# Performance work log

Measured on AMD Instinct MI355X. Metric: run time of the kernel, lower is better.

The kernel has to match this reference:

```python
import jax, jax.numpy as jnp
import numpy as np

N_USER, N_ENTITY, N_NEWS, N_REL, K, D, NNZ = 50000, 60000, 20000, 50, 20, 100, 500000

def setup_inputs() -> dict:
    key = jax.random.key(0)
    ks = jax.random.split(key, 12)
    return {
        "user_emb": jax.random.normal(ks[0], (N_USER, D), jnp.float32),
        "all_embedding": jax.random.normal(ks[1], (N_ENTITY, D), jnp.float32),
        "entity_emb": jax.random.normal(ks[2], (N_ENTITY, D), jnp.float32),
        "relation_emb": jax.random.normal(ks[3], (N_REL, D), jnp.float32),
        "W_news": jax.random.normal(ks[4], (D, 1), jnp.float32) * 0.1,
        "b_news": jax.random.normal(ks[5], (1,), jnp.float32) * 0.1,
        "W_ent": jax.random.normal(ks[6], (D, 1), jnp.float32) * 0.1,
        "b_ent": jax.random.normal(ks[7], (1,), jnp.float32) * 0.1,
        "interact_vals": jax.random.uniform(ks[8], (NNZ,), jnp.float32),
        "news_entities": jax.random.randint(ks[9], (N_NEWS, K), 0, N_ENTITY, jnp.int32),
        "news_relations": jnp.zeros((N_NEWS, K), jnp.int32),  # original code hardcodes relation 0 for news
        "neigh_entities": jax.random.randint(ks[10], (N_ENTITY, K), 0, N_ENTITY, jnp.int32),
        "neigh_relations": jax.random.randint(ks[11], (N_ENTITY, K), 0, N_REL, jnp.int32),
        "interact_rows": jax.random.randint(jax.random.fold_in(key, 100), (NNZ,), 0, N_USER, jnp.int32),
        "interact_cols": jax.random.randint(jax.random.fold_in(key, 101), (NNZ,), 0, N_NEWS + N_ENTITY, jnp.int32),
    }

def reference(user_emb, all_embedding, entity_emb, relation_emb, W_news, b_news,
              W_ent, b_ent, interact_vals, news_entities, news_relations,
              neigh_entities, neigh_relations, interact_rows, interact_cols):
    n_news = news_entities.shape[0]
    n_entity = entity_emb.shape[0]
    n_user = user_emb.shape[0]

    # --- news aggregation: newsid = arange(N_NEWS) ---
    news_emb = all_embedding[:n_news]                              # [N_news, D]
    nne = entity_emb[news_entities]                                # [N_news, K, D]
    nnr = relation_emb[news_relations]                             # [N_news, K, D]
    news_logits = (nne + nnr) @ W_news + b_news                    # [N_news, K, 1]
    # faithful: softmax over last (size-1) dim -> all-ones weights
    news_w = jax.nn.softmax(news_logits, axis=-1)
    news_agg = jnp.einsum('nko,nkd->nd', news_w, nne)              # [N_news, D]

    # --- entity aggregation: entities = arange(n_entity); entity_emb overwritten ---
    ent_base = all_embedding[:n_entity]                            # [n_entity, D]
    ne = ent_base[neigh_entities]                                  # [n_entity, K, D]
    nr = relation_emb[neigh_relations]                             # [n_entity, K, D]
    ent_logits = (nr + ne) @ W_ent + b_ent                         # [n_entity, K, 1]
    ent_w = jax.nn.softmax(ent_logits, axis=-1)
    entity_agg = jnp.einsum('nko,nkd->nd', ent_w, ne)              # [n_entity, D]

    node_emb = jnp.concatenate([news_agg + news_emb, entity_agg + ent_base], axis=0)

    # --- sparse mm: interact_mat [n_user, n_news+n_entity] in COO ---
    gathered = interact_vals[:, None] * node_emb[interact_cols]    # [nnz, D]
    user_agg = jax.ops.segment_sum(gathered, interact_rows, num_segments=n_user)
    user_agg = user_emb + user_agg
    return node_emb, user_agg
```

## Files before the change

### kernel.cpp

```cpp
#include <hip/hip_runtime.h>
#include <hip/hip_bf16.h>

constexpr int D        = 100;
constexpr int K        = 20;
constexpr int N_USER   = 50000;
constexpr int N_ENTITY = 60000;
constexpr int N_NEWS   = 20000;
constexpr int NNZ      = 500000;
constexpr int CAP      = 32;
constexpr int N_NODE   = N_NEWS + N_ENTITY;
constexpr int FS       = 32;

constexpr int PREP_WAVES = N_ENTITY;
constexpr int PREP_ROWT  = PREP_WAVES * 64;

__global__ __launch_bounds__(256) void prep_kernel(
    const float* __restrict__ ent, const float* __restrict__ all,
    unsigned int* __restrict__ entQ, unsigned int* __restrict__ allQ,
    int* __restrict__ counts, int* __restrict__ listcnt)
{
    int i = (int)(blockIdx.x * blockDim.x + threadIdx.x);
    if (i < PREP_ROWT) {
        int w    = i >> 6;
        int lane = i & 63;
        int li   = lane & 31;
        int sub  = lane >> 5;
        bool isEnt = w < PREP_WAVES / 2;
        const float* src = isEnt ? ent : all;
        unsigned int* dst = isEnt ? entQ : allQ;
        int row = 2 * (isEnt ? w : (w - PREP_WAVES / 2)) + sub;

        float v0 = 0.f, v1 = 0.f, v2 = 0.f, v3 = 0.f, lmax = 0.f;
        if (li < 25) {
            const float* sp = src + (size_t)row * D + li * 4;
            v0 = __builtin_nontemporal_load(sp + 0);
            v1 = __builtin_nontemporal_load(sp + 1);
            v2 = __builtin_nontemporal_load(sp + 2);
            v3 = __builtin_nontemporal_load(sp + 3);
            lmax = fmaxf(fmaxf(fabsf(v0), fabsf(v1)),
                         fmaxf(fabsf(v2), fabsf(v3)));
        }
        #pragma unroll
        for (int off = 16; off >= 1; off >>= 1)
            lmax = fmaxf(lmax, __shfl_xor(lmax, off));

        float inv = (lmax > 0.f) ? (127.0f / lmax) : 0.f;
        unsigned int o = 0;
        if (li < 25) {
            int q0 = (int)rintf(v0 * inv);
            int q1 = (int)rintf(v1 * inv);
            int q2 = (int)rintf(v2 * inv);
            int q3 = (int)rintf(v3 * inv);
            o = ((unsigned int)(unsigned char)(signed char)q0)
              | ((unsigned int)(unsigned char)(signed char)q1 << 8)
              | ((unsigned int)(unsigned char)(signed char)q2 << 16)
              | ((unsigned int)(unsigned char)(signed char)q3 << 24);
        } else if (li == 25) {
            o = __float_as_uint(lmax * (1.0f / 127.0f));
        }
        dst[(size_t)row * FS + li] = o;
    } else {
        int j = i - PREP_ROWT;
        if (j < N_USER) counts[j] = 0;
        else if (j == N_USER) *listcnt = 0;
    }
}

static __device__ __forceinline__ void sumagg_body(
    const unsigned int* __restrict__ tabQ,
    const int*   __restrict__ idx_mat,
    const float* __restrict__ base,
    float*       __restrict__ node,
    unsigned int* __restrict__ nodeQ,
    int pair, int lane)
{
    int li   = lane & 31;
    int sub  = lane >> 5;
    int row  = pair * 2 + sub;

    int idxv = (li < K)
        ? __builtin_nontemporal_load(idx_mat + (size_t)row * K + li) : 0;

    unsigned int t[K];
    #pragma unroll
    for (int k = 0; k < K; ++k) {
        int col = __shfl(idxv, sub * 32 + k);
        t[k] = tabQ[(size_t)col * FS + li];
    }

    float a0 = 0.f, a1 = 0.f, a2 = 0.f, a3 = 0.f;
    #pragma unroll
    for (int k = 0; k < K; ++k) {
        float sc = __uint_as_float((unsigned int)__shfl((int)t[k], sub * 32 + 25));
        unsigned int u = t[k];
        a0 += (float)((signed char)(u       & 0xFF)) * sc;
        a1 += (float)((signed char)((u >> 8) & 0xFF)) * sc;
        a2 += (float)((signed char)((u >> 16) & 0xFF)) * sc;
        a3 += (float)((int)u >> 24) * sc;
    }

    float o0 = 0.f, o1 = 0.f, o2 = 0.f, o3 = 0.f, lmax = 0.f;
    if (li < 25) {
        const float* bp = base + (size_t)row * D + li * 4;
        o0 = a0 + __builtin_nontemporal_load(bp + 0);
        o1 = a1 + __builtin_nontemporal_load(bp + 1);
        o2 = a2 + __builtin_nontemporal_load(bp + 2);
        o3 = a3 + __builtin_nontemporal_load(bp + 3);
        float* np = node + (size_t)row * D + li * 4;
        __builtin_nontemporal_store(o0, np + 0);
        __builtin_nontemporal_store(o1, np + 1);
        __builtin_nontemporal_store(o2, np + 2);
        __builtin_nontemporal_store(o3, np + 3);
        lmax = fmaxf(fmaxf(fabsf(o0), fabsf(o1)),
                     fmaxf(fabsf(o2), fabsf(o3)));
    }
    #pragma unroll
    for (int off = 16; off >= 1; off >>= 1)
        lmax = fmaxf(lmax, __shfl_xor(lmax, off));
    float inv = (lmax > 0.f) ? (127.0f / lmax) : 0.f;

    unsigned int oq = 0;
    if (li < 25) {
        int q0 = (int)rintf(o0 * inv);
        int q1 = (int)rintf(o1 * inv);
        int q2 = (int)rintf(o2 * inv);
        int q3 = (int)rintf(o3 * inv);
        oq = ((unsigned int)(unsigned char)(signed char)q0)
           | ((unsigned int)(unsigned char)(signed char)q1 << 8)
           | ((unsigned int)(unsigned char)(signed char)q2 << 16)
           | ((unsigned int)(unsigned char)(signed char)q3 << 24);
    } else if (li == 25) {
        oq = __float_as_uint(lmax * (1.0f / 127.0f));
    }
    nodeQ[(size_t)row * FS + li] = oq;
}

static __device__ __forceinline__ void hist_body(
    const int* __restrict__ rows, const int* __restrict__ cols,
    const float* __restrict__ vals,
    int* __restrict__ counts, unsigned int* __restrict__ bpack,
    int* __restrict__ list, int* __restrict__ listcnt, int j)
{
    int r   = __builtin_nontemporal_load(rows + j);
    int pos = atomicAdd(&counts[r], 1);
    if (pos < CAP) {
        int   c = __builtin_nontemporal_load(cols + j);
        float v = __builtin_nontemporal_load(vals + j);
        int q = (int)(v * 32767.0f + 0.5f);
        if (q > 32767) q = 32767;
        if (q < 0) q = 0;
        bpack[(size_t)r * CAP + pos] = (unsigned int)c | ((unsigned int)q << 17);
    } else {
        int s = atomicAdd(listcnt, 1);
        list[s] = j;
    }
}

constexpr int NEWS_BLK = (N_NEWS / 2 + 3) / 4;
constexpr int HIST_BLK = (NNZ + 255) / 256;

__global__ __launch_bounds__(256) void news_hist_kernel(
    const unsigned int* __restrict__ entQ,
    const int*   __restrict__ news_ent,
    const float* __restrict__ base,
    float*       __restrict__ node,
    unsigned int* __restrict__ nodeQ,
    const int* __restrict__ irows, const int* __restrict__ icols,
    const float* __restrict__ vals,
    int* __restrict__ counts, unsigned int* __restrict__ bpack,
    int* __restrict__ list, int* __restrict__ listcnt)
{
    int b = (int)blockIdx.x;
    if (b < NEWS_BLK) {
        int pair = b * 4 + (int)(threadIdx.x >> 6);
        if (pair < N_NEWS / 2)
            sumagg_body(entQ, news_ent, base, node, nodeQ,
                        pair, (int)threadIdx.x & 63);
    } else {
        int j = (b - NEWS_BLK) * 256 + (int)threadIdx.x;
        if (j < NNZ)
            hist_body(irows, icols, vals, counts, bpack, list, listcnt, j);
    }
}

__global__ __launch_bounds__(256) void sumagg_q8_kernel(
    const unsigned int* __restrict__ tabQ,
    const int*   __restrict__ idx_mat,
    const float* __restrict__ base,
    float*       __restrict__ node,
    unsigned int* __restrict__ nodeQ,
    int n)
{
    int pair = (int)((blockIdx.x * blockDim.x + threadIdx.x) >> 6);
    if (pair >= (n >> 1)) return;
    sumagg_body(tabQ, idx_mat, base, node, nodeQ,
                pair, (int)threadIdx.x & 63);
}

__global__ __launch_bounds__(256) void user_agg_q8_kernel(
    const int* __restrict__ counts, const unsigned int* __restrict__ bpack,
    const unsigned int* __restrict__ nodeQ,
    const float* __restrict__ user_emb, float* __restrict__ user)
{
    int u    = (int)((blockIdx.x * blockDim.x + threadIdx.x) >> 6);
    int lane = threadIdx.x & 63;
    int li   = lane & 31;
    int sub  = lane >> 5;
    if (u >= N_USER) return;

    int c = counts[u];
    if (c > CAP) c = CAP;

    int colv = 0; float valv = 0.f;
    if (lane < c) {
        unsigned int pk = __builtin_nontemporal_load(bpack + (size_t)u * CAP + lane);
        colv = (int)(pk & 0x1FFFFu);
        valv = (float)(pk >> 17) * (1.0f / 32767.0f);
    }
    int clampi = (c > 0) ? (c - 1) : 0;
    int pairs  = (c + 1) >> 1;

    float a0 = 0.f, a1 = 0.f, a2 = 0.f, a3 = 0.f;
    for (int p0 = 0; p0 < pairs; p0 += 4) {
        unsigned int t[4]; float v[4];
        #pragma unroll
        for (int e = 0; e < 4; ++e) {
            int pe    = 2 * (p0 + e) + sub;
            bool valid = pe < c;
            int es    = valid ? pe : clampi;
            int   col = __shfl(colv, es);
            float vv  = __shfl(valv, es);
            v[e] = valid ? vv : 0.f;
            t[e] = nodeQ[(size_t)col * FS + li];
        }
        #pragma unroll
        for (int e = 0; e < 4; ++e) {
            float sc = __uint_as_float(
                (unsigned int)__shfl((int)t[e], sub * 32 + 25)) * v[e];
            unsigned int w = t[e];
            a0 += (float)((signed char)(w       & 0xFF)) * sc;
            a1 += (float)((signed char)((w >> 8) & 0xFF)) * sc;
            a2 += (float)((signed char)((w >> 16) & 0xFF)) * sc;
            a3 += (float)((int)w >> 24) * sc;
        }
    }
    a0 += __shfl_xor(a0, 32);
    a1 += __shfl_xor(a1, 32);
    a2 += __shfl_xor(a2, 32);
    a3 += __shfl_xor(a3, 32);

    if (sub == 0 && li < 25) {
        const float* up = user_emb + (size_t)u * D + li * 4;
        float u0 = __builtin_nontemporal_load(up + 0);
        float u1 = __builtin_nontemporal_load(up + 1);
        float u2 = __builtin_nontemporal_load(up + 2);
        float u3 = __builtin_nontemporal_load(up + 3);
        float* op = user + (size_t)u * D + li * 4;
        __builtin_nontemporal_store(a0 + u0, op + 0);
        __builtin_nontemporal_store(a1 + u1, op + 1);
        __builtin_nontemporal_store(a2 + u2, op + 2);
        __builtin_nontemporal_store(a3 + u3, op + 3);
    }
}

__global__ __launch_bounds__(256) void drain_kernel(
    const int* __restrict__ list, const int* __restrict__ listcnt,
    const int* __restrict__ rows, const int* __restrict__ cols,
    const float* __restrict__ vals, const float* __restrict__ node,
    float* __restrict__ user)
{
    int nw   = (int)((gridDim.x * blockDim.x) >> 6);
    int wid  = (int)((blockIdx.x * blockDim.x + threadIdx.x) >> 6);
    int lane = threadIdx.x & 63;
    int cnt  = *listcnt;
    if (cnt > NNZ) cnt = NNZ;
    for (int s = wid; s < cnt; s += nw) {
        int j = list[s];
        int   r = rows[j];
        int   c = cols[j];
        float v = vals[j];
        const float* src = node + (size_t)c * D;
        float*       dst = user + (size_t)r * D;
        unsafeAtomicAdd(&dst[lane], v * src[lane]);
        int l2 = lane + 64;
        if (l2 < D) unsafeAtomicAdd(&dst[l2], v * src[l2]);
    }
}

__global__ __launch_bounds__(256) void zero2_kernel(
    int* __restrict__ counts, int* __restrict__ listcnt, int n)
{
    int i = (int)(blockIdx.x * blockDim.x + threadIdx.x);
    if (i < n) counts[i] = 0;
    else if (i == n) *listcnt = 0;
}

__global__ __launch_bounds__(256) void hist_fill_kernel(
    const int* __restrict__ rows, const int* __restrict__ cols,
    const float* __restrict__ vals,
    int* __restrict__ counts, unsigned int* __restrict__ bpack,
    int* __restrict__ list, int* __restrict__ listcnt, int nnz)
{
    int j = (int)(blockIdx.x * blockDim.x + threadIdx.x);
    if (j >= nnz) return;
    hist_body(rows, cols, vals, counts, bpack, list, listcnt, j);
}

__global__ __launch_bounds__(256) void sumagg_f32_kernel(
    const float* __restrict__ table, const int* __restrict__ idx_mat,
    const float* __restrict__ base, float* __restrict__ out, int n)
{
    int wave = (int)((blockIdx.x * blockDim.x + threadIdx.x) >> 6);
    int lane = threadIdx.x & 63;
    if (wave >= n) return;
    int idxv = (lane < K) ? idx_mat[(size_t)wave * K + lane] : 0;
    float acc0 = 0.f, acc1 = 0.f;
    int l2 = lane + 64;
    #pragma unroll
    for (int k = 0; k < K; ++k) {
        int ei = __shfl(idxv, k);
        const float* r = table + (size_t)ei * D;
        acc0 += r[lane];
        if (l2 < D) acc1 += r[l2];
    }
    const float* b = base + (size_t)wave * D;
    float*       o = out  + (size_t)wave * D;
    o[lane] = acc0 + b[lane];
    if (l2 < D) o[l2] = acc1 + b[l2];
}

__global__ __launch_bounds__(256) void user_agg_f32_kernel(
    const int* __restrict__ counts, const unsigned int* __restrict__ bpack,
    const float* __restrict__ node,
    const float* __restrict__ user_emb, float* __restrict__ user)
{
    int u    = (int)((blockIdx.x * blockDim.x + threadIdx.x) >> 6);
    int lane = threadIdx.x & 63;
    if (u >= N_USER) return;
    int c = counts[u];
    if (c > CAP) c = CAP;
    int colv = 0; float valv = 0.f;
    if (lane < c) {
        unsigned int pk = bpack[(size_t)u * CAP + lane];
        colv = (int)(pk & 0x1FFFFu);
        valv = (float)(pk >> 17) * (1.0f / 32767.0f);
    }
    float a0 = 0.f, a1 = 0.f;
    int l2 = lane + 64;
    for (int e = 0; e < c; ++e) {
        int   col = __shfl(colv, e);
        float v   = __shfl(valv, e);
        const float* r = node + (size_t)col * D;
        a0 += v * r[lane];
        if (l2 < D) a1 += v * r[l2];
    }
    const float* ue = user_emb + (size_t)u * D;
    float*       o  = user     + (size_t)u * D;
    o[lane] = a0 + ue[lane];
    if (l2 < D) o[l2] = a1 + ue[l2];
}

__global__ __launch_bounds__(256) void copy_kernel(
    const float4* __restrict__ src, float4* __restrict__ dst, int n4)
{
    int i = (int)(blockIdx.x * blockDim.x + threadIdx.x);
    if (i < n4) dst[i] = src[i];
}

__global__ __launch_bounds__(256) void scatter_kernel(
    const float* __restrict__ vals, const int* __restrict__ rows,
    const int* __restrict__ cols, const float* __restrict__ node,
    float* __restrict__ user, int nnz)
{
    int j    = (int)((blockIdx.x * blockDim.x + threadIdx.x) >> 6);
    int lane = threadIdx.x & 63;
    if (j >= nnz) return;
    int   r = rows[j];
    int   c = cols[j];
    float v = vals[j];
    const float* src = node + (size_t)c * D;
    float*       dst = user + (size_t)r * D;
    unsafeAtomicAdd(&dst[lane], v * src[lane]);
    int l2 = lane + 64;
    if (l2 < D) unsafeAtomicAdd(&dst[l2], v * src[l2]);
}

extern "C" void kernel_launch(void* const* d_in, const int* in_sizes, int n_in,
                              void* d_out, int out_size, void* d_ws, size_t ws_size,
                              hipStream_t stream)
{
    const float* user_emb = (const float*)d_in[0];
    const float* all_emb  = (const float*)d_in[1];
    const float* ent_emb  = (const float*)d_in[2];
    const float* vals     = (const float*)d_in[8];
    const int*   news_ent = (const int*)d_in[9];
    const int*   ngh_ent  = (const int*)d_in[11];
    const int*   irows    = (const int*)d_in[13];
    const int*   icols    = (const int*)d_in[14];

    float* node = (float*)d_out;
    float* user = (float*)d_out + (size_t)N_NODE * D;

    int*   counts  = (int*)d_ws;
    int*   list    = counts + N_USER;
    int*   listcnt = list + NNZ;
    unsigned int* bpack = (unsigned int*)(listcnt + 64);
    unsigned int* entQ  = bpack + (size_t)N_USER * CAP;
    unsigned int* allQ  = entQ + (size_t)N_ENTITY * FS;
    unsigned int* nodeQ = allQ + (size_t)N_ENTITY * FS;

    size_t need_bucket = ((size_t)N_USER + NNZ + 64 + (size_t)N_USER * CAP) * 4ull;
    size_t need_full   = need_bucket
                       + (2ull * N_ENTITY + N_NODE) * FS * 4ull;

    if (ws_size >= need_full) {
        int prep_n = PREP_ROWT + N_USER + 1;
        prep_kernel<<<(prep_n + 255) / 256, 256, 0, stream>>>(
            ent_emb, all_emb, entQ, allQ, counts, listcnt);

        news_hist_kernel<<<NEWS_BLK + HIST_BLK, 256, 0, stream>>>(
            entQ, news_ent, all_emb, node, nodeQ,
            irows, icols, vals, counts, bpack, list, listcnt);

        sumagg_q8_kernel<<<(N_ENTITY / 2 + 3) / 4, 256, 0, stream>>>(
            allQ, ngh_ent, all_emb, node + (size_t)N_NEWS * D,
            nodeQ + (size_t)N_NEWS * FS, N_ENTITY);

        user_agg_q8_kernel<<<(N_USER + 3) / 4, 256, 0, stream>>>(
            counts, bpack, nodeQ, user_emb, user);
        drain_kernel<<<64, 256, 0, stream>>>(
            list, listcnt, irows, icols, vals, node, user);
    } else if (ws_size >= need_bucket) {
        sumagg_f32_kernel<<<(N_NEWS + 3) / 4, 256, 0, stream>>>(
            ent_emb, news_ent, all_emb, node, N_NEWS);
        sumagg_f32_kernel<<<(N_ENTITY + 3) / 4, 256, 0, stream>>>(
            all_emb, ngh_ent, all_emb, node + (size_t)N_NEWS * D, N_ENTITY);
        zero2_kernel<<<(N_USER + 256) / 256, 256, 0, stream>>>(
            counts, listcnt, N_USER);
        hist_fill_kernel<<<(NNZ + 255) / 256, 256, 0, stream>>>(
            irows, icols, vals, counts, bpack, list, listcnt, NNZ);
        user_agg_f32_kernel<<<(N_USER + 3) / 4, 256, 0, stream>>>(
            counts, bpack, node, user_emb, user);
        drain_kernel<<<64, 256, 0, stream>>>(
            list, listcnt, irows, icols, vals, node, user);
    } else {
        sumagg_f32_kernel<<<(N_NEWS + 3) / 4, 256, 0, stream>>>(
            ent_emb, news_ent, all_emb, node, N_NEWS);
        sumagg_f32_kernel<<<(N_ENTITY + 3) / 4, 256, 0, stream>>>(
            all_emb, ngh_ent, all_emb, node + (size_t)N_NEWS * D, N_ENTITY);
        int n4 = N_USER * D / 4;
        copy_kernel<<<(n4 + 255) / 256, 256, 0, stream>>>(
            (const float4*)user_emb, (float4*)user, n4);
        scatter_kernel<<<(NNZ + 3) / 4, 256, 0, stream>>>(
            vals, irows, icols, node, user, NNZ);
    }
}
```

Before: 128.5 us.

## Fuse entity aggregation into news/hist kernel and batch histogram loads per thread

Merges the entity-neighbour aggregation launch into the combined news-aggregation/histogram kernel, giving one launch with three block roles. Histogram blocks now come first, and each thread loads four COO entries up front before issuing its atomics, which exposes more memory-level parallelism. The aim is to remove one kernel launch and its inter-kernel gap and let the atomic-heavy histogram overlap with the gather-heavy aggregations. In exchange, histogram blocks are fewer and larger, and the same block-role scheduling can leave a tail of imbalanced work.

```diff
diff --git a/kernel.cpp b/kernel.cpp
--- a/kernel.cpp
+++ b/kernel.cpp
@@ -135,34 +135,17 @@
     nodeQ[(size_t)row * FS + li] = oq;
 }
 
-static __device__ __forceinline__ void hist_body(
-    const int* __restrict__ rows, const int* __restrict__ cols,
-    const float* __restrict__ vals,
-    int* __restrict__ counts, unsigned int* __restrict__ bpack,
-    int* __restrict__ list, int* __restrict__ listcnt, int j)
-{
-    int r   = __builtin_nontemporal_load(rows + j);
-    int pos = atomicAdd(&counts[r], 1);
-    if (pos < CAP) {
-        int   c = __builtin_nontemporal_load(cols + j);
-        float v = __builtin_nontemporal_load(vals + j);
-        int q = (int)(v * 32767.0f + 0.5f);
-        if (q > 32767) q = 32767;
-        if (q < 0) q = 0;
-        bpack[(size_t)r * CAP + pos] = (unsigned int)c | ((unsigned int)q << 17);
-    } else {
-        int s = atomicAdd(listcnt, 1);
-        list[s] = j;
-    }
-}
-
+constexpr int HIST_EPT = 4;
+constexpr int HIST_BLK = (NNZ + 256 * HIST_EPT - 1) / (256 * HIST_EPT);
+constexpr int ENT_BLK  = (N_ENTITY / 2 + 3) / 4;
 constexpr int NEWS_BLK = (N_NEWS / 2 + 3) / 4;
-constexpr int HIST_BLK = (NNZ + 255) / 256;
-
-__global__ __launch_bounds__(256) void news_hist_kernel(
+
+__global__ __launch_bounds__(256) void fused_kernel(
     const unsigned int* __restrict__ entQ,
+    const unsigned int* __restrict__ allQ,
     const int*   __restrict__ news_ent,
-    const float* __restrict__ base,
+    const int*   __restrict__ ngh_ent,
+    const float* __restrict__ all_emb,
     float*       __restrict__ node,
     unsigned int* __restrict__ nodeQ,
     const int* __restrict__ irows, const int* __restrict__ icols,
@@ -171,30 +154,46 @@
     int* __restrict__ list, int* __restrict__ listcnt)
 {
     int b = (int)blockIdx.x;
-    if (b < NEWS_BLK) {
-        int pair = b * 4 + (int)(threadIdx.x >> 6);
-        if (pair < N_NEWS / 2)
-            sumagg_body(entQ, news_ent, base, node, nodeQ,
+    if (b < HIST_BLK) {
+        int j0 = b * (256 * HIST_EPT) + (int)threadIdx.x;
+        int   r[HIST_EPT], cc[HIST_EPT];
+        float vv[HIST_EPT];
+        #pragma unroll
+        for (int e = 0; e < HIST_EPT; ++e) {
+            int j = j0 + e * 256;
+            bool ok = j < NNZ;
+            r[e]  = ok ? __builtin_nontemporal_load(irows + j) : -1;
+            cc[e] = ok ? __builtin_nontemporal_load(icols + j) : 0;
+            vv[e] = ok ? __builtin_nontemporal_load(vals  + j) : 0.f;
+        }
+        #pragma unroll
+        for (int e = 0; e < HIST_EPT; ++e) {
+            if (r[e] < 0) continue;
+            int pos = atomicAdd(&counts[r[e]], 1);
+            if (pos < CAP) {
+                int q = (int)(vv[e] * 32767.0f + 0.5f);
+                if (q > 32767) q = 32767;
+                if (q < 0) q = 0;
+                bpack[(size_t)r[e] * CAP + pos] =
+                    (unsigned int)cc[e] | ((unsigned int)q << 17);
+            } else {
+                int s = atomicAdd(listcnt, 1);
+                list[s] = j0 + e * 256;
+            }
+        }
+    } else if (b < HIST_BLK + ENT_BLK) {
+        int pair = (b - HIST_BLK) * 4 + (int)(threadIdx.x >> 6);
+        if (pair < N_ENTITY / 2)
+            sumagg_body(allQ, ngh_ent, all_emb,
+                        node + (size_t)N_NEWS * D,
+                        nodeQ + (size_t)N_NEWS * FS,
                         pair, (int)threadIdx.x & 63);
     } else {
-        int j = (b - NEWS_BLK) * 256 + (int)threadIdx.x;
-        if (j < NNZ)
-            hist_body(irows, icols, vals, counts, bpack, list, listcnt, j);
-    }
-}
-
-__global__ __launch_bounds__(256) void sumagg_q8_kernel(
-    const unsigned int* __restrict__ tabQ,
-    const int*   __restrict__ idx_mat,
-    const float* __restrict__ base,
-    float*       __restrict__ node,
-    unsigned int* __restrict__ nodeQ,
-    int n)
-{
-    int pair = (int)((blockIdx.x * blockDim.x + threadIdx.x) >> 6);
-    if (pair >= (n >> 1)) return;
-    sumagg_body(tabQ, idx_mat, base, node, nodeQ,
-                pair, (int)threadIdx.x & 63);
+        int pair = (b - HIST_BLK - ENT_BLK) * 4 + (int)(threadIdx.x >> 6);
+        if (pair < N_NEWS / 2)
+            sumagg_body(entQ, news_ent, all_emb, node, nodeQ,
+                        pair, (int)threadIdx.x & 63);
+    }
 }
 
 __global__ __launch_bounds__(256) void user_agg_q8_kernel(
@@ -303,7 +302,19 @@
 {
     int j = (int)(blockIdx.x * blockDim.x + threadIdx.x);
     if (j >= nnz) return;
-    hist_body(rows, cols, vals, counts, bpack, list, listcnt, j);
+    int r   = __builtin_nontemporal_load(rows + j);
+    int pos = atomicAdd(&counts[r], 1);
+    if (pos < CAP) {
+        int   c = __builtin_nontemporal_load(cols + j);
+        float v = __builtin_nontemporal_load(vals + j);
+        int q = (int)(v * 32767.0f + 0.5f);
+        if (q > 32767) q = 32767;
+        if (q < 0) q = 0;
+        bpack[(size_t)r * CAP + pos] = (unsigned int)c | ((unsigned int)q << 17);
+    } else {
+        int s = atomicAdd(listcnt, 1);
+        list[s] = j;
+    }
 }
 
 __global__ __launch_bounds__(256) void sumagg_f32_kernel(
@@ -418,13 +429,9 @@
         prep_kernel<<<(prep_n + 255) / 256, 256, 0, stream>>>(
             ent_emb, all_emb, entQ, allQ, counts, listcnt);
 
-        news_hist_kernel<<<NEWS_BLK + HIST_BLK, 256, 0, stream>>>(
-            entQ, news_ent, all_emb, node, nodeQ,
+        fused_kernel<<<HIST_BLK + ENT_BLK + NEWS_BLK, 256, 0, stream>>>(
+            entQ, allQ, news_ent, ngh_ent, all_emb, node, nodeQ,
             irows, icols, vals, counts, bpack, list, listcnt);
-
-        sumagg_q8_kernel<<<(N_ENTITY / 2 + 3) / 4, 256, 0, stream>>>(
-            allQ, ngh_ent, all_emb, node + (size_t)N_NEWS * D,
-            nodeQ + (size_t)N_NEWS * FS, N_ENTITY);
 
         user_agg_q8_kernel<<<(N_USER + 3) / 4, 256, 0, stream>>>(
             counts, bpack, nodeQ, user_emb, user);
```

Result: faster. 120.8 us (-6.0%).
